# Optimization experiments

Measured on AMD Instinct MI355X. Metric: run time of the kernel, lower is better.

## Reference

```python
import jax, jax.numpy as jnp
import numpy as np

N_NODES = 100000
N_EDGES = 1600000
IN_DIM = 128
HIDDEN = 128
OUT_DIM = 64


def setup_inputs() -> dict:
    key = jax.random.key(0)
    k_x, k_e, k_w1, k_b1, k_w2, k_b2 = jax.random.split(key, 6)
    x = jax.random.normal(k_x, (N_NODES, IN_DIM), dtype=jnp.float32)
    edge_index = jax.random.randint(k_e, (2, N_EDGES), 0, N_NODES, dtype=jnp.int64)
    # GCNConv weight/bias (glorot-ish scale) and final Linear head
    W1 = jax.random.normal(k_w1, (IN_DIM, HIDDEN), dtype=jnp.float32) / np.sqrt(IN_DIM)
    b1 = jnp.zeros((HIDDEN,), dtype=jnp.float32)
    W2 = jax.random.normal(k_w2, (HIDDEN, OUT_DIM), dtype=jnp.float32) / np.sqrt(HIDDEN)
    b2 = jnp.zeros((OUT_DIM,), dtype=jnp.float32)
    return {"x": x, "W1": W1, "b1": b1, "W2": W2, "b2": b2, "edge_index": edge_index}


def _gcn_conv(x, W, b, src, dst, norm, n_nodes):
    # PyG GCNConv: linear transform, then sym-normalized neighbor aggregation
    h = x @ W                                   # (N, H) dense transform
    msg = h[src] * norm[:, None]                # (E+N, H) gather + scale
    out = jax.ops.segment_sum(msg, dst, num_segments=n_nodes)  # scatter-add
    return out + b


def reference(x, W1, b1, W2, b2, edge_index):
    n = x.shape[0]
    # add self-loops (PyG GCNConv default)
    loop = jnp.arange(n, dtype=edge_index.dtype)
    src = jnp.concatenate([edge_index[0], loop])
    dst = jnp.concatenate([edge_index[1], loop])
    # symmetric normalization D^{-1/2} A D^{-1/2}
    deg = jnp.zeros((n,), dtype=x.dtype).at[dst].add(1.0)
    dinv = jnp.where(deg > 0, jax.lax.rsqrt(jnp.maximum(deg, 1.0)), 0.0)
    norm = dinv[src] * dinv[dst]

    h = _gcn_conv(x, W1, b1, src, dst, norm, n)
    h = jax.nn.relu(h)
    # dropout: identity in eval/inference mode
    return h @ W2 + b2
```

## Files before the change

### kernel.cpp

```cpp
#include <hip/hip_runtime.h>

#define N_NODES 100000
#define N_EDGES 1600000
#define IN_DIM  128
#define HIDDEN  128
#define OUT_DIM 64

#define NB_COARSE ((N_NODES + 255) / 256)
#define EPB 4096
#define NBLK_E ((N_EDGES + EPB - 1) / EPB)
#define GB1 ((N_NODES + 127) / 128)
#define CAP 5120
#define PCAP 6912

typedef __attribute__((ext_vector_type(8))) short bf8_t;
typedef __attribute__((ext_vector_type(4))) float f4_t;

__device__ __forceinline__ ushort f2b(float f) {
    unsigned int u = __float_as_uint(f);
    u += 0x7fffu + ((u >> 16) & 1u);
    return (ushort)(u >> 16);
}
__device__ __forceinline__ float b2f_lo(unsigned int u) { return __uint_as_float(u << 16); }
__device__ __forceinline__ float b2f_hi(unsigned int u) { return __uint_as_float(u & 0xffff0000u); }


__global__ __launch_bounds__(256, 2) void k_fuse1(const int* __restrict__ ei,
                                                  int* __restrict__ cursor,
                                                  unsigned int* __restrict__ part,
                                                  const float* __restrict__ x,
                                                  const float* __restrict__ W1,
                                                  ushort* __restrict__ h) {
    __shared__ __align__(16) ushort smem[2 * 128 * 136];
    int tid = threadIdx.x;

    if (blockIdx.x < NBLK_E) {
        int* lh    = (int*)smem;
        int* lbase = lh + NB_COARSE;
        for (int i = tid; i < NB_COARSE; i += 256) lh[i] = 0;
        __syncthreads();
        int e0 = blockIdx.x * EPB;
        int srcv[EPB / 256], dstv[EPB / 256];
        #pragma unroll
        for (int j = 0; j < EPB / 256; j++) {
            int e = e0 + j * 256 + tid;
            if (e < N_EDGES) {
                srcv[j] = ei[e];
                dstv[j] = ei[N_EDGES + e];
                atomicAdd(&lh[dstv[j] >> 8], 1);
            } else dstv[j] = -1;
        }
        __syncthreads();
        for (int i = tid; i < NB_COARSE; i += 256) {
            int c = lh[i];
            lbase[i] = (c > 0) ? (i * CAP + atomicAdd(&cursor[i], c)) : 0;
            lh[i] = 0;
        }
        __syncthreads();
        #pragma unroll
        for (int j = 0; j < EPB / 256; j++) {
            if (dstv[j] >= 0) {
                int b = dstv[j] >> 8;
                int pos = lbase[b] + atomicAdd(&lh[b], 1);
                part[pos] = ((unsigned int)(dstv[j] & 255) << 24) | (unsigned int)srcv[j];
            }
        }
        return;
    }

    typedef ushort (*tile_t)[136];
    tile_t As = (tile_t)smem;
    tile_t Bs = (tile_t)(smem + 128 * 136);
    int row0 = (blockIdx.x - NBLK_E) * 128;
    const int M = N_NODES;

    #pragma unroll
    for (int i = 0; i < 16; i++) {
        int li = tid + i * 256;
        int r = li >> 5, c4 = li & 31;
        int grow = row0 + r; if (grow > M - 1) grow = M - 1;
        float4 v = *(const float4*)(x + (size_t)grow * 128 + c4 * 4);
        ushort4 o;
        o.x = f2b(v.x); o.y = f2b(v.y); o.z = f2b(v.z); o.w = f2b(v.w);
        *(ushort4*)&As[r][c4 * 4] = o;
    }
    #pragma unroll
    for (int i = 0; i < 16; i++) {
        int li = tid + i * 256;
        int k = li >> 5, n4 = li & 31;
        float4 v = *(const float4*)(W1 + (size_t)k * 128 + n4 * 4);
        Bs[n4 * 4 + 0][k] = f2b(v.x);
        Bs[n4 * 4 + 1][k] = f2b(v.y);
        Bs[n4 * 4 + 2][k] = f2b(v.z);
        Bs[n4 * 4 + 3][k] = f2b(v.w);
    }
    __syncthreads();

    int wave = tid >> 6, lane = tid & 63;
    int lr = lane & 15, lq = lane >> 4;
    int wm0 = (wave & 1) * 64;
    int wn0 = (wave >> 1) * 64;

    f4_t acc[4][4];
    #pragma unroll
    for (int mi = 0; mi < 4; mi++)
        #pragma unroll
        for (int ni = 0; ni < 4; ni++) acc[mi][ni] = (f4_t){0.f, 0.f, 0.f, 0.f};

    #pragma unroll
    for (int kb = 0; kb < 4; kb++) {
        bf8_t af[4], bfr[4];
        #pragma unroll
        for (int mi = 0; mi < 4; mi++)
            af[mi] = *(const bf8_t*)&As[wm0 + mi * 16 + lr][kb * 32 + lq * 8];
        #pragma unroll
        for (int ni = 0; ni < 4; ni++)
            bfr[ni] = *(const bf8_t*)&Bs[wn0 + ni * 16 + lr][kb * 32 + lq * 8];
        #pragma unroll
        for (int mi = 0; mi < 4; mi++)
            #pragma unroll
            for (int ni = 0; ni < 4; ni++)
                acc[mi][ni] = __builtin_amdgcn_mfma_f32_16x16x32_bf16(
                    af[mi], bfr[ni], acc[mi][ni], 0, 0, 0);
    }

    #pragma unroll
    for (int mi = 0; mi < 4; mi++) {
        #pragma unroll
        for (int r = 0; r < 4; r++) {
            int row = row0 + wm0 + mi * 16 + lq * 4 + r;
            if (row < M) {
                #pragma unroll
                for (int ni = 0; ni < 4; ni++)
                    h[(size_t)row * 128 + wn0 + ni * 16 + lr] = f2b(acc[mi][ni][r]);
            }
        }
    }
}


__global__ __launch_bounds__(256) void k_csr(const unsigned int* __restrict__ part,
                                             const int* __restrict__ cursor,
                                             int* __restrict__ offs,
                                             int* __restrict__ pcnt,
                                             float* __restrict__ dinv,
                                             int* __restrict__ ssrc) {
    __shared__ int ldeg[256], lsc[256], lcur[256], sob[256];
    __shared__ unsigned int stage[CAP];
    int t = threadIdx.x;
    int b = blockIdx.x;
    int rbeg = b * CAP;
    int cnt = cursor[b];
    int node0 = b << 8;
    if (b == 0 && t == 0) dinv[N_NODES] = 0.f;
    ldeg[t] = 0;
    __syncthreads();
    for (int i = t; i < cnt; i += 256) {
        unsigned int u = part[rbeg + i];
        stage[i] = u;
        atomicAdd(&ldeg[u >> 24], 1);
    }
    __syncthreads();
    int v = ldeg[t];
    int pv = (v + 7) & ~7;
    lsc[t] = pv;
    __syncthreads();
    for (int off = 1; off < 256; off <<= 1) {
        int add = (t >= off) ? lsc[t - off] : 0;
        __syncthreads();
        lsc[t] += add;
        __syncthreads();
    }
    int ob = b * PCAP + (lsc[t] - pv);
    sob[t] = ob;
    lcur[t] = 0;
    if (node0 + t < N_NODES) {
        offs[node0 + t] = ob;
        pcnt[node0 + t] = pv;
        dinv[node0 + t] = rsqrtf((float)(v + 1));
    }
    __syncthreads();
    for (int i = t; i < cnt; i += 256) {
        unsigned int u = stage[i];
        int d = u >> 24;
        int pos = atomicAdd(&lcur[d], 1);
        ssrc[sob[d] + pos] = (int)(u & 0xFFFFFFu);
    }
    for (int i = v; i < pv; i++) ssrc[ob + i] = N_NODES;
}


__global__ __launch_bounds__(256, 6) void k_agg2(const ushort* __restrict__ h,
                                                 const int* __restrict__ offs,
                                                 const int* __restrict__ pcnt,
                                                 const int* __restrict__ ssrc,
                                                 const float* __restrict__ dinv,
                                                 const float* __restrict__ b1,
                                                 const float* __restrict__ W2,
                                                 const float* __restrict__ b2,
                                                 float* __restrict__ out) {
    __shared__ ushort As[16][136];
    __shared__ ushort Bs[64][136];
    int tid = threadIdx.x;
    int wave = tid >> 6, lane = tid & 63;
    int base = blockIdx.x * 16;

    #pragma unroll
    for (int i = 0; i < 8; i++) {
        int li = tid + i * 256;
        int k = li >> 4, n4 = li & 15;
        float4 v = *(const float4*)(W2 + (size_t)k * 64 + n4 * 4);
        Bs[n4 * 4 + 0][k] = f2b(v.x);
        Bs[n4 * 4 + 1][k] = f2b(v.y);
        Bs[n4 * 4 + 2][k] = f2b(v.z);
        Bs[n4 * 4 + 3][k] = f2b(v.w);
    }

    const unsigned int* hp = (const unsigned int*)h;
    float2 bb = ((const float2*)b1)[lane];

    #pragma unroll 1
    for (int j = 0; j < 4; j++) {
        int r = wave * 4 + j;
        int n = base + r;
        int e0 = offs[n];
        int iters = pcnt[n] >> 3;
        const uint4* ip = (const uint4*)(ssrc + e0);

        float ax0 = 0.f, ay0 = 0.f, ax1 = 0.f, ay1 = 0.f;
        float ax2 = 0.f, ay2 = 0.f, ax3 = 0.f, ay3 = 0.f;
        uint4 i0, i1;
        if (iters > 0) { i0 = ip[0]; i1 = ip[1]; }
        for (int it = 0; it < iters; it++) {
            uint4 nx0 = i0, nx1 = i1;
            if (it + 1 < iters) { nx0 = ip[(it + 1) * 2]; nx1 = ip[(it + 1) * 2 + 1]; }
            float w0 = dinv[i0.x], w1 = dinv[i0.y], w2 = dinv[i0.z], w3 = dinv[i0.w];
            float w4 = dinv[i1.x], w5 = dinv[i1.y], w6 = dinv[i1.z], w7 = dinv[i1.w];
            unsigned int u0 = hp[i0.x * 64 + lane];
            unsigned int u1 = hp[i0.y * 64 + lane];
            unsigned int u2 = hp[i0.z * 64 + lane];
            unsigned int u3 = hp[i0.w * 64 + lane];
            unsigned int u4 = hp[i1.x * 64 + lane];
            unsigned int u5 = hp[i1.y * 64 + lane];
            unsigned int u6 = hp[i1.z * 64 + lane];
            unsigned int u7 = hp[i1.w * 64 + lane];
            ax0 = fmaf(b2f_lo(u0), w0, ax0); ay0 = fmaf(b2f_hi(u0), w0, ay0);
            ax1 = fmaf(b2f_lo(u1), w1, ax1); ay1 = fmaf(b2f_hi(u1), w1, ay1);
            ax2 = fmaf(b2f_lo(u2), w2, ax2); ay2 = fmaf(b2f_hi(u2), w2, ay2);
            ax3 = fmaf(b2f_lo(u3), w3, ax3); ay3 = fmaf(b2f_hi(u3), w3, ay3);
            ax0 = fmaf(b2f_lo(u4), w4, ax0); ay0 = fmaf(b2f_hi(u4), w4, ay0);
            ax1 = fmaf(b2f_lo(u5), w5, ax1); ay1 = fmaf(b2f_hi(u5), w5, ay1);
            ax2 = fmaf(b2f_lo(u6), w6, ax2); ay2 = fmaf(b2f_hi(u6), w6, ay2);
            ax3 = fmaf(b2f_lo(u7), w7, ax3); ay3 = fmaf(b2f_hi(u7), w7, ay3);
            i0 = nx0; i1 = nx1;
        }
        unsigned int us = hp[(size_t)n * 64 + lane];
        float dn = dinv[n];
        float rx = (ax0 + ax1 + ax2 + ax3 + b2f_lo(us) * dn) * dn + bb.x;
        float ry = (ay0 + ay1 + ay2 + ay3 + b2f_hi(us) * dn) * dn + bb.y;
        rx = rx > 0.f ? rx : 0.f;
        ry = ry > 0.f ? ry : 0.f;
        *(unsigned int*)&As[r][lane * 2] =
            ((unsigned int)f2b(ry) << 16) | (unsigned int)f2b(rx);
    }
    __syncthreads();

    int lr = lane & 15, lq = lane >> 4;
    f4_t acc = (f4_t){0.f, 0.f, 0.f, 0.f};
    #pragma unroll
    for (int kb = 0; kb < 4; kb++) {
        bf8_t af = *(const bf8_t*)&As[lr][kb * 32 + lq * 8];
        bf8_t bf = *(const bf8_t*)&Bs[wave * 16 + lr][kb * 32 + lq * 8];
        acc = __builtin_amdgcn_mfma_f32_16x16x32_bf16(af, bf, acc, 0, 0, 0);
    }
    int col = wave * 16 + lr;
    float bv = b2[col];
    #pragma unroll
    for (int r = 0; r < 4; r++) {
        int node = base + lq * 4 + r;
        out[(size_t)node * 64 + col] = acc[r] + bv;
    }
}


extern "C" void kernel_launch(void* const* d_in, const int* in_sizes, int n_in,
                              void* d_out, int out_size, void* d_ws, size_t ws_size,
                              hipStream_t stream) {
    const float* x  = (const float*)d_in[0];
    const float* W1 = (const float*)d_in[1];
    const float* b1 = (const float*)d_in[2];
    const float* W2 = (const float*)d_in[3];
    const float* b2 = (const float*)d_in[4];
    const int*   ei = (const int*)d_in[5];
    float* out = (float*)d_out;

    char* w = (char*)d_ws;
    size_t off = 0;
    auto alloc = [&](size_t bytes) -> void* {
        void* p = w + off;
        off += (bytes + 255) & ~(size_t)255;
        return p;
    };
    ushort* h      = (ushort*)alloc((size_t)(N_NODES + 1) * HIDDEN * 2);
    float* dinv    = (float*)alloc((size_t)(N_NODES + 1) * 4);
    int*   offs    = (int*)alloc((size_t)N_NODES * 4);
    int*   pcnt    = (int*)alloc((size_t)N_NODES * 4);
    int*   ssrc    = (int*)alloc((size_t)NB_COARSE * PCAP * 4);
    unsigned int* part = (unsigned int*)alloc((size_t)NB_COARSE * CAP * 4);
    int*   cursor  = (int*)alloc((size_t)NB_COARSE * 4);

    hipMemsetAsync(cursor, 0, (size_t)NB_COARSE * 4, stream);
    k_fuse1<<<NBLK_E + GB1, 256, 0, stream>>>(ei, cursor, part, x, W1, h);
    k_csr<<<NB_COARSE, 256, 0, stream>>>(part, cursor, offs, pcnt, dinv, ssrc);
    k_agg2<<<N_NODES / 16, 256, 0, stream>>>(h, offs, pcnt, ssrc, dinv, b1, W2, b2, out);
}
```

Before: 220.5 us.

## Use finer 64-node buckets for CSR build and scalarize gather indices

```diff
diff --git a/kernel.cpp b/kernel.cpp
--- a/kernel.cpp
+++ b/kernel.cpp
@@ -6,12 +6,14 @@
 #define HIDDEN  128
 #define OUT_DIM 64
 
-#define NB_COARSE ((N_NODES + 255) / 256)
+#define BUCK_SHIFT 6
+#define BUCK_SZ    64
+#define NB_BUCK ((N_NODES + BUCK_SZ - 1) / BUCK_SZ)
 #define EPB 4096
 #define NBLK_E ((N_EDGES + EPB - 1) / EPB)
 #define GB1 ((N_NODES + 127) / 128)
-#define CAP 5120
-#define PCAP 6912
+#define CAP 1536
+#define PCAP 1984
 
 typedef __attribute__((ext_vector_type(8))) short bf8_t;
 typedef __attribute__((ext_vector_type(4))) float f4_t;
@@ -36,8 +38,8 @@
 
     if (blockIdx.x < NBLK_E) {
         int* lh    = (int*)smem;
-        int* lbase = lh + NB_COARSE;
-        for (int i = tid; i < NB_COARSE; i += 256) lh[i] = 0;
+        int* lbase = lh + NB_BUCK;
+        for (int i = tid; i < NB_BUCK; i += 256) lh[i] = 0;
         __syncthreads();
         int e0 = blockIdx.x * EPB;
         int srcv[EPB / 256], dstv[EPB / 256];
@@ -47,11 +49,11 @@
             if (e < N_EDGES) {
                 srcv[j] = ei[e];
                 dstv[j] = ei[N_EDGES + e];
-                atomicAdd(&lh[dstv[j] >> 8], 1);
+                atomicAdd(&lh[dstv[j] >> BUCK_SHIFT], 1);
             } else dstv[j] = -1;
         }
         __syncthreads();
-        for (int i = tid; i < NB_COARSE; i += 256) {
+        for (int i = tid; i < NB_BUCK; i += 256) {
             int c = lh[i];
             lbase[i] = (c > 0) ? (i * CAP + atomicAdd(&cursor[i], c)) : 0;
             lh[i] = 0;
@@ -60,9 +62,9 @@
         #pragma unroll
         for (int j = 0; j < EPB / 256; j++) {
             if (dstv[j] >= 0) {
-                int b = dstv[j] >> 8;
+                int b = dstv[j] >> BUCK_SHIFT;
                 int pos = lbase[b] + atomicAdd(&lh[b], 1);
-                part[pos] = ((unsigned int)(dstv[j] & 255) << 24) | (unsigned int)srcv[j];
+                part[pos] = ((unsigned int)(dstv[j] & (BUCK_SZ - 1)) << 24) | (unsigned int)srcv[j];
             }
         }
         return;
@@ -144,16 +146,20 @@
                                              int* __restrict__ offs,
                                              int* __restrict__ pcnt,
                                              float* __restrict__ dinv,
-                                             int* __restrict__ ssrc) {
-    __shared__ int ldeg[256], lsc[256], lcur[256], sob[256];
+                                             int* __restrict__ ssrc,
+                                             ushort* __restrict__ h) {
+    __shared__ int ldeg[BUCK_SZ], lsc[BUCK_SZ], lcur[BUCK_SZ], sob[BUCK_SZ];
     __shared__ unsigned int stage[CAP];
     int t = threadIdx.x;
     int b = blockIdx.x;
     int rbeg = b * CAP;
     int cnt = cursor[b];
-    int node0 = b << 8;
-    if (b == 0 && t == 0) dinv[N_NODES] = 0.f;
-    ldeg[t] = 0;
+    int node0 = b << BUCK_SHIFT;
+    if (b == 0) {
+        if (t == 0) dinv[N_NODES] = 0.f;
+        if (t < 128) h[(size_t)N_NODES * 128 + t] = 0;
+    }
+    if (t < BUCK_SZ) ldeg[t] = 0;
     __syncthreads();
     for (int i = t; i < cnt; i += 256) {
         unsigned int u = part[rbeg + i];
@@ -161,23 +167,29 @@
         atomicAdd(&ldeg[u >> 24], 1);
     }
     __syncthreads();
-    int v = ldeg[t];
-    int pv = (v + 7) & ~7;
-    lsc[t] = pv;
-    __syncthreads();
-    for (int off = 1; off < 256; off <<= 1) {
-        int add = (t >= off) ? lsc[t - off] : 0;
-        __syncthreads();
-        lsc[t] += add;
-        __syncthreads();
-    }
-    int ob = b * PCAP + (lsc[t] - pv);
-    sob[t] = ob;
-    lcur[t] = 0;
-    if (node0 + t < N_NODES) {
-        offs[node0 + t] = ob;
-        pcnt[node0 + t] = pv;
-        dinv[node0 + t] = rsqrtf((float)(v + 1));
+    int v = 0, pv = 0;
+    if (t < BUCK_SZ) {
+        v = ldeg[t];
+        pv = (v + 7) & ~7;
+        lsc[t] = pv;
+    }
+    __syncthreads();
+    for (int off = 1; off < BUCK_SZ; off <<= 1) {
+        int add = 0;
+        if (t < BUCK_SZ && t >= off) add = lsc[t - off];
+        __syncthreads();
+        if (t < BUCK_SZ) lsc[t] += add;
+        __syncthreads();
+    }
+    if (t < BUCK_SZ) {
+        int ob = b * PCAP + (lsc[t] - pv);
+        sob[t] = ob;
+        lcur[t] = 0;
+        if (node0 + t < N_NODES) {
+            offs[node0 + t] = ob;
+            pcnt[node0 + t] = pv;
+            dinv[node0 + t] = rsqrtf((float)(v + 1));
+        }
     }
     __syncthreads();
     for (int i = t; i < cnt; i += 256) {
@@ -186,11 +198,12 @@
         int pos = atomicAdd(&lcur[d], 1);
         ssrc[sob[d] + pos] = (int)(u & 0xFFFFFFu);
     }
-    for (int i = v; i < pv; i++) ssrc[ob + i] = N_NODES;
-}
-
-
-__global__ __launch_bounds__(256, 6) void k_agg2(const ushort* __restrict__ h,
+    if (t < BUCK_SZ)
+        for (int i = v; i < pv; i++) ssrc[sob[t] + i] = N_NODES;
+}
+
+
+__global__ __launch_bounds__(256, 7) void k_agg2(const ushort* __restrict__ h,
                                                  const int* __restrict__ offs,
                                                  const int* __restrict__ pcnt,
                                                  const int* __restrict__ ssrc,
@@ -223,8 +236,8 @@
     for (int j = 0; j < 4; j++) {
         int r = wave * 4 + j;
         int n = base + r;
-        int e0 = offs[n];
-        int iters = pcnt[n] >> 3;
+        int e0 = __builtin_amdgcn_readfirstlane(offs[n]);
+        int iters = __builtin_amdgcn_readfirstlane(pcnt[n]) >> 3;
         const uint4* ip = (const uint4*)(ssrc + e0);
 
         float ax0 = 0.f, ay0 = 0.f, ax1 = 0.f, ay1 = 0.f;
@@ -234,16 +247,24 @@
         for (int it = 0; it < iters; it++) {
             uint4 nx0 = i0, nx1 = i1;
             if (it + 1 < iters) { nx0 = ip[(it + 1) * 2]; nx1 = ip[(it + 1) * 2 + 1]; }
-            float w0 = dinv[i0.x], w1 = dinv[i0.y], w2 = dinv[i0.z], w3 = dinv[i0.w];
-            float w4 = dinv[i1.x], w5 = dinv[i1.y], w6 = dinv[i1.z], w7 = dinv[i1.w];
-            unsigned int u0 = hp[i0.x * 64 + lane];
-            unsigned int u1 = hp[i0.y * 64 + lane];
-            unsigned int u2 = hp[i0.z * 64 + lane];
-            unsigned int u3 = hp[i0.w * 64 + lane];
-            unsigned int u4 = hp[i1.x * 64 + lane];
-            unsigned int u5 = hp[i1.y * 64 + lane];
-            unsigned int u6 = hp[i1.z * 64 + lane];
-            unsigned int u7 = hp[i1.w * 64 + lane];
+            int s0 = __builtin_amdgcn_readfirstlane((int)i0.x);
+            int s1 = __builtin_amdgcn_readfirstlane((int)i0.y);
+            int s2 = __builtin_amdgcn_readfirstlane((int)i0.z);
+            int s3 = __builtin_amdgcn_readfirstlane((int)i0.w);
+            int s4 = __builtin_amdgcn_readfirstlane((int)i1.x);
+            int s5 = __builtin_amdgcn_readfirstlane((int)i1.y);
+            int s6 = __builtin_amdgcn_readfirstlane((int)i1.z);
+            int s7 = __builtin_amdgcn_readfirstlane((int)i1.w);
+            unsigned int u0 = (hp + ((unsigned)s0 << 6))[lane];
+            unsigned int u1 = (hp + ((unsigned)s1 << 6))[lane];
+            unsigned int u2 = (hp + ((unsigned)s2 << 6))[lane];
+            unsigned int u3 = (hp + ((unsigned)s3 << 6))[lane];
+            unsigned int u4 = (hp + ((unsigned)s4 << 6))[lane];
+            unsigned int u5 = (hp + ((unsigned)s5 << 6))[lane];
+            unsigned int u6 = (hp + ((unsigned)s6 << 6))[lane];
+            unsigned int u7 = (hp + ((unsigned)s7 << 6))[lane];
+            float w0 = dinv[s0], w1 = dinv[s1], w2 = dinv[s2], w3 = dinv[s3];
+            float w4 = dinv[s4], w5 = dinv[s5], w6 = dinv[s6], w7 = dinv[s7];
             ax0 = fmaf(b2f_lo(u0), w0, ax0); ay0 = fmaf(b2f_hi(u0), w0, ay0);
             ax1 = fmaf(b2f_lo(u1), w1, ax1); ay1 = fmaf(b2f_hi(u1), w1, ay1);
             ax2 = fmaf(b2f_lo(u2), w2, ax2); ay2 = fmaf(b2f_hi(u2), w2, ay2);
@@ -305,12 +326,12 @@
     float* dinv    = (float*)alloc((size_t)(N_NODES + 1) * 4);
     int*   offs    = (int*)alloc((size_t)N_NODES * 4);
     int*   pcnt    = (int*)alloc((size_t)N_NODES * 4);
-    int*   ssrc    = (int*)alloc((size_t)NB_COARSE * PCAP * 4);
-    unsigned int* part = (unsigned int*)alloc((size_t)NB_COARSE * CAP * 4);
-    int*   cursor  = (int*)alloc((size_t)NB_COARSE * 4);
-
-    hipMemsetAsync(cursor, 0, (size_t)NB_COARSE * 4, stream);
+    int*   ssrc    = (int*)alloc((size_t)NB_BUCK * PCAP * 4);
+    unsigned int* part = (unsigned int*)alloc((size_t)NB_BUCK * CAP * 4);
+    int*   cursor  = (int*)alloc((size_t)NB_BUCK * 4);
+
+    hipMemsetAsync(cursor, 0, (size_t)NB_BUCK * 4, stream);
     k_fuse1<<<NBLK_E + GB1, 256, 0, stream>>>(ei, cursor, part, x, W1, h);
-    k_csr<<<NB_COARSE, 256, 0, stream>>>(part, cursor, offs, pcnt, dinv, ssrc);
+    k_csr<<<NB_BUCK, 256, 0, stream>>>(part, cursor, offs, pcnt, dinv, ssrc, h);
     k_agg2<<<N_NODES / 16, 256, 0, stream>>>(h, offs, pcnt, ssrc, dinv, b1, W2, b2, out);
 }
```

After: 217.5 us. No clear change (-1.4%).
